# Performance work log

Measured on AMD Instinct MI355X. Metric: run time of the kernel, lower is better.

## Reference

```python
import jax, jax.numpy as jnp
import numpy as np

B, C, H, W = 8, 128, 64, 64


def setup_inputs() -> dict:
    key = jax.random.key(0)
    ks = jax.random.split(key, 7)
    query_img = jax.random.normal(ks[0], (B, C, H, W), dtype=jnp.float32)
    key_img = jax.random.normal(ks[1], (B, C, H, W), dtype=jnp.float32)
    value_img = jax.random.normal(ks[2], (B, C, H, W), dtype=jnp.float32)
    # 1x1 conv weights == dense [out, in] matrices (kaiming-ish scale)
    scale = 1.0 / np.sqrt(C)
    Wq = jax.random.normal(ks[3], (C, C), dtype=jnp.float32) * scale
    bq = jax.random.normal(ks[4], (C,), dtype=jnp.float32) * scale
    Wk = jax.random.normal(ks[5], (C, C), dtype=jnp.float32) * scale
    bk = jax.random.normal(ks[6], (C,), dtype=jnp.float32) * scale
    return {"query_img": query_img, "key_img": key_img, "value_img": value_img,
            "Wq": Wq, "bq": bq, "Wk": Wk, "bk": bk}


def reference(query_img, key_img, value_img, Wq, bq, Wk, bk):
    b, c, h, w = query_img.shape
    hw = h * w
    # 1x1 convs as GEMMs -> token-major layout (b, hw, c_out)
    q = jnp.einsum('bchw,oc->bhwo', query_img, Wq).reshape(b, hw, -1) + bq
    k = jnp.einsum('bchw,oc->bohw', key_img, Wk).reshape(b, -1, hw) + bk[None, :, None]
    # scores scaled by sqrt(HW) (faithful: key.size(-1) == h*w in source)
    scores = jnp.einsum('bqc,bck->bqk', q, k) / jnp.sqrt(jnp.float32(hw))
    attn = jax.nn.softmax(scores, axis=-1)  # (b, hw, hw)
    v = value_img.reshape(b, c, hw).transpose(0, 2, 1)  # (b, hw, c)
    out = jnp.einsum('bqk,bkc->bqc', attn, v)  # (b, hw, c)
    out = out.transpose(0, 2, 1).reshape(b, -1, h, w)
    out = out + q.transpose(0, 2, 1).reshape(b, -1, h, w)  # residual from query proj
    return out
```

## Files before the change

### kernel.cpp

```cpp
#include <hip/hip_runtime.h>

#define BB 8
#define CC 128
#define SS 4096
#define KT 64
#define SCALE 0.015625f

typedef __attribute__((ext_vector_type(8))) short sh8;
typedef __attribute__((ext_vector_type(4))) float f32x4;

__device__ __forceinline__ float b2f(unsigned short u) {
    union { unsigned int i; float f; } x; x.i = ((unsigned int)u) << 16; return x.f;
}
__device__ __forceinline__ unsigned short f2b(float f) {
    union { float f; unsigned int i; } x; x.f = f;
    unsigned int r = x.i + 0x7fff + ((x.i >> 16) & 1);
    return (unsigned short)(r >> 16);
}

__device__ __forceinline__ void dma16(const void* g, void* l) {
    __builtin_amdgcn_global_load_lds((const __attribute__((address_space(1))) void*)g,
                                     (__attribute__((address_space(3))) void*)l,
                                     16, 0, 0);
}

__global__ __launch_bounds__(256) void cvt_kernel(
    const float* __restrict__ vimg,
    const float* __restrict__ Wq, const float* __restrict__ Wk,
    const float* __restrict__ bq, const float* __restrict__ bk,
    unsigned short* __restrict__ Vbuf,
    unsigned short* __restrict__ Wqb, unsigned short* __restrict__ Wkb,
    unsigned short* __restrict__ bqb, unsigned short* __restrict__ bkb)
{
    const int bx = blockIdx.x, tid = threadIdx.x;
    if (bx < 512) {
        const size_t base = (size_t)bx * 8192 + tid * 4;
        #pragma unroll
        for (int it = 0; it < 8; ++it) {
            const size_t i = base + (size_t)it * 1024;
            float4 v = *(const float4*)(vimg + i);
            ushort4 o;
            o.x = f2b(v.x); o.y = f2b(v.y); o.z = f2b(v.z); o.w = f2b(v.w);
            *(ushort4*)(Vbuf + i) = o;
        }
    } else {
        const int w = bx - 512;
        for (int e = w * 256 + tid; e < 33024; e += 2048) {
            float v; unsigned short* dst;
            if (e < 16384)      { v = Wq[e];         dst = Wqb + e; }
            else if (e < 32768) { v = Wk[e - 16384]; dst = Wkb + (e - 16384); }
            else if (e < 32896) { v = bq[e - 32768]; dst = bqb + (e - 32768); }
            else                { v = bk[e - 32896]; dst = bkb + (e - 32896); }
            *dst = f2b(v);
        }
    }
}

__global__ __launch_bounds__(256) void proj_kernel(
    const float* __restrict__ qimg, const float* __restrict__ kimg,
    const unsigned short* __restrict__ Wqb, const unsigned short* __restrict__ Wkb,
    const unsigned short* __restrict__ bqb, const unsigned short* __restrict__ bkb,
    unsigned short* __restrict__ Qbuf, unsigned short* __restrict__ Kbuf)
{
    const int z = blockIdx.z;
    const float* img = (z == 0) ? qimg : kimg;
    const unsigned short* Wb = (z == 0) ? Wqb : Wkb;
    const unsigned short* bias = (z == 0) ? bqb : bkb;
    unsigned short* outTok = (z == 0) ? Qbuf : Kbuf;

    const int tid  = threadIdx.x;
    const int wave = tid >> 6;
    const int lane = tid & 63;
    const int l15  = lane & 15;
    const int quad = lane >> 4;
    const int b     = blockIdx.y;
    const int stile = blockIdx.x;
    const int sbase = stile * 64 + wave * 16;

    sh8 a[4];
    {
        const float* ip = img + (size_t)b * CC * SS + (sbase + l15);
        #pragma unroll
        for (int kk = 0; kk < 4; ++kk)
            #pragma unroll
            for (int j = 0; j < 8; ++j)
                a[kk][j] = (short)f2b(ip[(size_t)(32 * kk + quad * 8 + j) * SS]);
    }

    f32x4 acc[8];
    #pragma unroll
    for (int nt = 0; nt < 8; ++nt) acc[nt] = (f32x4){0.f, 0.f, 0.f, 0.f};

    #pragma unroll
    for (int nt = 0; nt < 8; ++nt) {
        const unsigned short* wp = Wb + (size_t)(16 * nt + l15) * CC + quad * 8;
        #pragma unroll
        for (int kk = 0; kk < 4; ++kk) {
            sh8 bf = *(const sh8*)(wp + 32 * kk);
            acc[nt] = __builtin_amdgcn_mfma_f32_16x16x32_bf16(a[kk], bf, acc[nt], 0, 0, 0);
        }
    }

    #pragma unroll
    for (int nt = 0; nt < 8; ++nt) {
        const int o = 16 * nt + l15;
        const float bv = b2f(bias[o]);
        #pragma unroll
        for (int r = 0; r < 4; ++r) {
            const int s = stile * 64 + wave * 16 + quad * 4 + r;
            outTok[((size_t)b * SS + s) * CC + o] = f2b(acc[nt][r] + bv);
        }
    }
}

__global__ __launch_bounds__(256) void attn_kernel(
    const unsigned short* __restrict__ Qbuf,
    const unsigned short* __restrict__ Kbuf,
    const unsigned short* __restrict__ Vbuf,
    float* __restrict__ out)
{
    __shared__ __align__(16) unsigned char smem[58368];
    unsigned char* kb0 = smem;
    unsigned char* kb1 = smem + 16384;
    unsigned char* vb  = smem + 32768;

    const int tid  = threadIdx.x;
    const int wave = tid >> 6;
    const int lane = tid & 63;
    const int l15  = lane & 15;
    const int quad = lane >> 4;
    const int b     = blockIdx.y;
    const int qtile = blockIdx.x;
    const int qbase = qtile * 64 + wave * 16;

    unsigned short* pw = (unsigned short*)(smem + 49152) + wave * 16 * 72;

    const unsigned short* kbp = Kbuf + (size_t)b * SS * CC;
    const unsigned short* vbp = Vbuf + (size_t)b * CC * SS;

    sh8 aq[4];
    {
        const unsigned short* qp = Qbuf + ((size_t)b * SS + qbase + l15) * CC + quad * 8;
        #pragma unroll
        for (int kk = 0; kk < 4; ++kk) aq[kk] = *(const sh8*)(qp + 32 * kk);
    }

    int kGO[4], vGO[4];
    #pragma unroll
    for (int j = 0; j < 4; ++j) {
        const int krow = wave * 16 + j * 4 + (lane >> 4);
        kGO[j] = krow * 256 + (((lane & 15) ^ (krow & 7)) << 4);
        const int vrow = (wave * 4 + j) * 8 + (lane >> 3);
        vGO[j] = vrow * 8192 + (((lane & 7) ^ ((lane >> 3) & 7)) << 4);
    }

    f32x4 oacc[8];
    #pragma unroll
    for (int ct = 0; ct < 8; ++ct) oacc[ct] = (f32x4){0.f, 0.f, 0.f, 0.f};
    float lsum[4] = {0.f, 0.f, 0.f, 0.f};

    {
        const char* gk = (const char*)kbp;
        const char* gv = (const char*)vbp;
        #pragma unroll
        for (int j = 0; j < 4; ++j) {
            dma16(gk + kGO[j], kb0 + (wave * 4 + j) * 1024);
            dma16(gv + vGO[j], vb  + (wave * 4 + j) * 1024);
        }
    }
    __syncthreads();

    for (int it = 0; it < SS / KT; ++it) {
        const int kt0 = it * KT;
        unsigned char* kb  = (it & 1) ? kb1 : kb0;
        unsigned char* kbn = (it & 1) ? kb0 : kb1;

        if (it + 1 < SS / KT) {
            const char* gk = (const char*)kbp + (size_t)(kt0 + KT) * 256;
            #pragma unroll
            for (int j = 0; j < 4; ++j)
                dma16(gk + kGO[j], kbn + (wave * 4 + j) * 1024);
        }
        if (it > 0) {
            const char* gv = (const char*)vbp + (size_t)kt0 * 2;
            #pragma unroll
            for (int j = 0; j < 4; ++j)
                dma16(gv + vGO[j], vb + (wave * 4 + j) * 1024);
        }

        f32x4 sacc[4];
        #pragma unroll
        for (int n = 0; n < 4; ++n) {
            sacc[n] = (f32x4){0.f, 0.f, 0.f, 0.f};
            #pragma unroll
            for (int kk = 0; kk < 4; ++kk) {
                sh8 kf = *(const sh8*)(kb + (16 * n + l15) * 256
                                          + (((4 * kk + quad) ^ (l15 & 7)) << 4));
                sacc[n] = __builtin_amdgcn_mfma_f32_16x16x32_bf16(aq[kk], kf, sacc[n], 0, 0, 0);
            }
        }

        #pragma unroll
        for (int n = 0; n < 4; ++n)
            #pragma unroll
            for (int r = 0; r < 4; ++r) {
                float p = __expf(sacc[n][r] * SCALE);
                unsigned short pb16 = f2b(p);
                lsum[r] += b2f(pb16);
                pw[(quad * 4 + r) * 72 + 16 * n + l15] = pb16;
            }

        __syncthreads();

        #pragma unroll
        for (int ks = 0; ks < 2; ++ks) {
            sh8 ap = *(const sh8*)((const unsigned char*)pw
                                   + l15 * 144 + (32 * ks + quad * 8) * 2);
            #pragma unroll
            for (int ct = 0; ct < 8; ++ct) {
                sh8 bv = *(const sh8*)(vb + (16 * ct + l15) * 128
                                          + (((4 * ks + quad) ^ (l15 & 7)) << 4));
                oacc[ct] = __builtin_amdgcn_mfma_f32_16x16x32_bf16(ap, bv, oacc[ct], 0, 0, 0);
            }
        }

        __syncthreads();
    }

    #pragma unroll
    for (int r = 0; r < 4; ++r) {
        float v = lsum[r];
        #pragma unroll
        for (int m = 8; m >= 1; m >>= 1) v += __shfl_xor(v, m, 64);
        lsum[r] = v;
    }

    float (*oLds)[129] = (float(*)[129])smem;
    #pragma unroll
    for (int ct = 0; ct < 8; ++ct) {
        const int c = 16 * ct + l15;
        #pragma unroll
        for (int r = 0; r < 4; ++r) {
            const int qloc  = wave * 16 + quad * 4 + r;
            const int qglob = qtile * 64 + qloc;
            const float resid = b2f(Qbuf[((size_t)b * SS + qglob) * CC + c]);
            oLds[qloc][c] = oacc[ct][r] / lsum[r] + resid;
        }
    }
    __syncthreads();
    for (int idx = tid; idx < 64 * 128; idx += 256) {
        const int c = idx >> 6, q = idx & 63;
        out[((size_t)b * CC + c) * SS + qtile * 64 + q] = oLds[q][c];
    }
}

extern "C" void kernel_launch(void* const* d_in, const int* in_sizes, int n_in,
                              void* d_out, int out_size, void* d_ws, size_t ws_size,
                              hipStream_t stream) {
    const float* qimg = (const float*)d_in[0];
    const float* kimg = (const float*)d_in[1];
    const float* vimg = (const float*)d_in[2];
    const float* Wq   = (const float*)d_in[3];
    const float* bq   = (const float*)d_in[4];
    const float* Wk   = (const float*)d_in[5];
    const float* bk   = (const float*)d_in[6];
    float* out = (float*)d_out;

    unsigned short* Qbuf = (unsigned short*)d_ws;
    unsigned short* Kbuf = Qbuf + (size_t)BB * SS * CC;
    unsigned short* Vbuf = Kbuf + (size_t)BB * SS * CC;
    unsigned short* Wqb  = Vbuf + (size_t)BB * SS * CC;
    unsigned short* Wkb  = Wqb + CC * CC;
    unsigned short* bqb  = Wkb + CC * CC;
    unsigned short* bkb  = bqb + CC;

    cvt_kernel<<<dim3(520), 256, 0, stream>>>(vimg, Wq, Wk, bq, bk,
                                              Vbuf, Wqb, Wkb, bqb, bkb);
    proj_kernel<<<dim3(SS / 64, BB, 2), 256, 0, stream>>>(
        qimg, kimg, Wqb, Wkb, bqb, bkb, Qbuf, Kbuf);
    attn_kernel<<<dim3(SS / 64, BB), 256, 0, stream>>>(Qbuf, Kbuf, Vbuf, out);
}
```

Baseline: 225.8 us.

## Cut attention LDS to single buffer for higher occupancy and stage projection input through LDS

The attention kernel drops double-buffered K for a single K/V buffer, shrinking LDS from about 57KB to 40KB, and requests four blocks per CU via launch bounds. The next tile's DMA now starts after the second half of V and P has been read into registers, so it overlaps the final MFMAs. The P tile uses a 128-byte row layout with an XOR swizzle, the row sum is kept in fp32, and bf16 rounding becomes round-half-up. The projection kernel loads its input tile with coalesced float4 reads into LDS instead of strided scalar global loads. The trade-off is less prefetch depth per block, and the rounding change shifts numerics slightly.

Result: no change. 224.8 us (-0.4%).

```diff
diff --git a/kernel.cpp b/kernel.cpp
--- a/kernel.cpp
+++ b/kernel.cpp
@@ -16,6 +16,10 @@
     union { float f; unsigned int i; } x; x.f = f;
     unsigned int r = x.i + 0x7fff + ((x.i >> 16) & 1);
     return (unsigned short)(r >> 16);
+}
+__device__ __forceinline__ unsigned short rhu(float f) {
+    union { float f; unsigned int i; } x; x.f = f;
+    return (unsigned short)((x.i + 0x8000) >> 16);
 }
 
 __device__ __forceinline__ void dma16(const void* g, void* l) {
@@ -62,6 +66,8 @@
     const unsigned short* __restrict__ bqb, const unsigned short* __restrict__ bkb,
     unsigned short* __restrict__ Qbuf, unsigned short* __restrict__ Kbuf)
 {
+    __shared__ float ilds[128 * 69];
+
     const int z = blockIdx.z;
     const float* img = (z == 0) ? qimg : kimg;
     const unsigned short* Wb = (z == 0) ? Wqb : Wkb;
@@ -75,17 +81,25 @@
     const int quad = lane >> 4;
     const int b     = blockIdx.y;
     const int stile = blockIdx.x;
-    const int sbase = stile * 64 + wave * 16;
-
+
+    const float* gbase = img + (size_t)b * CC * SS + stile * 64;
+    #pragma unroll
+    for (int i = 0; i < 8; ++i) {
+        const int l = tid + 256 * i;
+        const int row = l >> 4, col = (l & 15) * 4;
+        float4 v = *(const float4*)(gbase + (size_t)row * SS + col);
+        float* d = ilds + row * 69 + col;
+        d[0] = v.x; d[1] = v.y; d[2] = v.z; d[3] = v.w;
+    }
+    __syncthreads();
+
+    const int tcol = wave * 16 + l15;
     sh8 a[4];
-    {
-        const float* ip = img + (size_t)b * CC * SS + (sbase + l15);
-        #pragma unroll
-        for (int kk = 0; kk < 4; ++kk)
-            #pragma unroll
-            for (int j = 0; j < 8; ++j)
-                a[kk][j] = (short)f2b(ip[(size_t)(32 * kk + quad * 8 + j) * SS]);
-    }
+    #pragma unroll
+    for (int kk = 0; kk < 4; ++kk)
+        #pragma unroll
+        for (int j = 0; j < 8; ++j)
+            a[kk][j] = (short)rhu(ilds[(32 * kk + quad * 8 + j) * 69 + tcol]);
 
     f32x4 acc[8];
     #pragma unroll
@@ -113,16 +127,15 @@
     }
 }
 
-__global__ __launch_bounds__(256) void attn_kernel(
+__global__ __launch_bounds__(256, 4) void attn_kernel(
     const unsigned short* __restrict__ Qbuf,
     const unsigned short* __restrict__ Kbuf,
     const unsigned short* __restrict__ Vbuf,
     float* __restrict__ out)
 {
-    __shared__ __align__(16) unsigned char smem[58368];
-    unsigned char* kb0 = smem;
-    unsigned char* kb1 = smem + 16384;
-    unsigned char* vb  = smem + 32768;
+    __shared__ __align__(16) unsigned char smem[40960];
+    unsigned char* kb = smem;
+    unsigned char* vb = smem + 16384;
 
     const int tid  = threadIdx.x;
     const int wave = tid >> 6;
@@ -133,7 +146,7 @@
     const int qtile = blockIdx.x;
     const int qbase = qtile * 64 + wave * 16;
 
-    unsigned short* pw = (unsigned short*)(smem + 49152) + wave * 16 * 72;
+    unsigned char* pw = smem + 32768 + wave * 2048;
 
     const unsigned short* kbp = Kbuf + (size_t)b * SS * CC;
     const unsigned short* vbp = Vbuf + (size_t)b * CC * SS;
@@ -159,34 +172,14 @@
     for (int ct = 0; ct < 8; ++ct) oacc[ct] = (f32x4){0.f, 0.f, 0.f, 0.f};
     float lsum[4] = {0.f, 0.f, 0.f, 0.f};
 
-    {
-        const char* gk = (const char*)kbp;
-        const char* gv = (const char*)vbp;
-        #pragma unroll
-        for (int j = 0; j < 4; ++j) {
-            dma16(gk + kGO[j], kb0 + (wave * 4 + j) * 1024);
-            dma16(gv + vGO[j], vb  + (wave * 4 + j) * 1024);
-        }
-    }
-    __syncthreads();
+    #pragma unroll
+    for (int j = 0; j < 4; ++j) {
+        dma16((const char*)kbp + kGO[j], kb + (wave * 4 + j) * 1024);
+        dma16((const char*)vbp + vGO[j], vb + (wave * 4 + j) * 1024);
+    }
 
     for (int it = 0; it < SS / KT; ++it) {
-        const int kt0 = it * KT;
-        unsigned char* kb  = (it & 1) ? kb1 : kb0;
-        unsigned char* kbn = (it & 1) ? kb0 : kb1;
-
-        if (it + 1 < SS / KT) {
-            const char* gk = (const char*)kbp + (size_t)(kt0 + KT) * 256;
-            #pragma unroll
-            for (int j = 0; j < 4; ++j)
-                dma16(gk + kGO[j], kbn + (wave * 4 + j) * 1024);
-        }
-        if (it > 0) {
-            const char* gv = (const char*)vbp + (size_t)kt0 * 2;
-            #pragma unroll
-            for (int j = 0; j < 4; ++j)
-                dma16(gv + vGO[j], vb + (wave * 4 + j) * 1024);
-        }
+        __syncthreads();
 
         f32x4 sacc[4];
         #pragma unroll
@@ -205,26 +198,43 @@
             #pragma unroll
             for (int r = 0; r < 4; ++r) {
                 float p = __expf(sacc[n][r] * SCALE);
-                unsigned short pb16 = f2b(p);
-                lsum[r] += b2f(pb16);
-                pw[(quad * 4 + r) * 72 + 16 * n + l15] = pb16;
+                lsum[r] += p;
+                const int row = quad * 4 + r, col = 16 * n + l15;
+                *(unsigned short*)(pw + row * 128
+                                   + (((col >> 3) ^ (row & 7)) << 4)
+                                   + (col & 7) * 2) = rhu(p);
             }
 
+        sh8 ap0 = *(const sh8*)(pw + l15 * 128 + ((quad ^ (l15 & 7)) << 4));
+        #pragma unroll
+        for (int ct = 0; ct < 8; ++ct) {
+            sh8 bv = *(const sh8*)(vb + (16 * ct + l15) * 128
+                                      + ((quad ^ (l15 & 7)) << 4));
+            oacc[ct] = __builtin_amdgcn_mfma_f32_16x16x32_bf16(ap0, bv, oacc[ct], 0, 0, 0);
+        }
+
+        sh8 ap1 = *(const sh8*)(pw + l15 * 128 + (((4 + quad) ^ (l15 & 7)) << 4));
+        sh8 vv[8];
+        #pragma unroll
+        for (int ct = 0; ct < 8; ++ct)
+            vv[ct] = *(const sh8*)(vb + (16 * ct + l15) * 128
+                                      + (((4 + quad) ^ (l15 & 7)) << 4));
+
         __syncthreads();
 
-        #pragma unroll
-        for (int ks = 0; ks < 2; ++ks) {
-            sh8 ap = *(const sh8*)((const unsigned char*)pw
-                                   + l15 * 144 + (32 * ks + quad * 8) * 2);
+        if (it + 1 < SS / KT) {
+            const char* gk = (const char*)kbp + (size_t)(it + 1) * KT * 256;
+            const char* gv = (const char*)vbp + (size_t)(it + 1) * KT * 2;
             #pragma unroll
-            for (int ct = 0; ct < 8; ++ct) {
-                sh8 bv = *(const sh8*)(vb + (16 * ct + l15) * 128
-                                          + (((4 * ks + quad) ^ (l15 & 7)) << 4));
-                oacc[ct] = __builtin_amdgcn_mfma_f32_16x16x32_bf16(ap, bv, oacc[ct], 0, 0, 0);
+            for (int j = 0; j < 4; ++j) {
+                dma16(gk + kGO[j], kb + (wave * 4 + j) * 1024);
+                dma16(gv + vGO[j], vb + (wave * 4 + j) * 1024);
             }
         }
 
-        __syncthreads();
+        #pragma unroll
+        for (int ct = 0; ct < 8; ++ct)
+            oacc[ct] = __builtin_amdgcn_mfma_f32_16x16x32_bf16(ap1, vv[ct], oacc[ct], 0, 0, 0);
     }
 
     #pragma unroll
```
